# Kernel optimization log

Measured on AMD Instinct MI355X. Metric: run time of the kernel, lower is better.

Reference implementation:

```python
import jax, jax.numpy as jnp
import numpy as np

EPS = 1e-5

def _layernorm(x, g, b):
    m = jnp.mean(x, axis=-1, keepdims=True)
    v = jnp.var(x, axis=-1, keepdims=True)
    return (x - m) * jax.lax.rsqrt(v + EPS) * g + b

def setup_inputs() -> dict:
    key = jax.random.key(0)
    ks = jax.random.split(key, 8)
    B, N, D, H = 4, 2048, 1024, 16
    F = 2 * D
    s = 0.02
    return {
        "x": jax.random.normal(ks[0], (B, N, D), jnp.float32),
        "mask": jnp.zeros((B, N, N), jnp.float32),
        "Wq": jax.random.normal(ks[1], (D, D), jnp.float32) * s,
        "Wk": jax.random.normal(ks[2], (D, D), jnp.float32) * s,
        "Wv": jax.random.normal(ks[3], (D, D), jnp.float32) * s,
        "Wc": jax.random.normal(ks[4], (D, D), jnp.float32) * s,
        "bc": jnp.zeros((D,), jnp.float32),
        "W1": jax.random.normal(ks[5], (D, F), jnp.float32) * s,
        "b1": jnp.zeros((F,), jnp.float32),
        "W2": jax.random.normal(ks[6], (F, D), jnp.float32) * s,
        "b2": jnp.zeros((D,), jnp.float32),
        "g1": jnp.ones((D,), jnp.float32),
        "be1": jnp.zeros((D,), jnp.float32),
        "g2": jnp.ones((D,), jnp.float32),
        "be2": jnp.zeros((D,), jnp.float32),
    }

def reference(x, mask, Wq, Wk, Wv, Wc, bc, W1, b1, W2, b2, g1, be1, g2, be2):
    B, N, D = x.shape
    H = 16
    Dh = D // H
    scale = 1.0 / np.sqrt(Dh).astype(np.float32)
    # projections -> [B, H, N, Dh]
    def heads(t):
        return t.reshape(B, N, H, Dh).transpose(0, 2, 1, 3)
    q = heads(x @ Wq)
    k = heads(x @ Wk)
    v = heads(x @ Wv)
    score = jnp.einsum('bhnd,bhmd->bhnm', q, k) * scale + mask[:, None, :, :]
    attn = jnp.einsum('bhnm,bhmd->bhnd', jax.nn.softmax(score, axis=-1), v)
    attn = attn.transpose(0, 2, 1, 3).reshape(B, N, D)
    x = x + attn @ Wc + bc
    x = _layernorm(x, g1, be1)
    x = x + jnp.maximum(x @ W1 + b1, 0.0) @ W2 + b2
    x = _layernorm(x, g2, be2)
    return x
```

## Files before the change

kernel.cpp:

```cpp
#include <hip/hip_runtime.h>
#include <hip/hip_bf16.h>


#define DEV __device__ __forceinline__

using s16x8 = __attribute__((ext_vector_type(8))) short;
using f32x4 = __attribute__((ext_vector_type(4))) float;

DEV unsigned short f2bf(float f) {
  unsigned u = __float_as_uint(f);
  u += 0x7fffu + ((u >> 16) & 1u);
  return (unsigned short)(u >> 16);
}
DEV unsigned pack2bf(float a, float b) {
  return (unsigned)f2bf(a) | ((unsigned)f2bf(b) << 16);
}
DEV unsigned cvt_pk_bf16(float lo, float hi) {
  unsigned r;
  asm("v_cvt_pk_bf16_f32 %0, %1, %2" : "=v"(r) : "v"(lo), "v"(hi));
  return r;
}
DEV f32x4 vmax4(f32x4 a, f32x4 b) {
  f32x4 r;
  r[0] = fmaxf(a[0], b[0]); r[1] = fmaxf(a[1], b[1]);
  r[2] = fmaxf(a[2], b[2]); r[3] = fmaxf(a[3], b[3]);
  return r;
}

typedef __attribute__((address_space(3))) unsigned lds_u32_t;
typedef const __attribute__((address_space(1))) unsigned glb_u32_t;

DEV void gld_lds16(const void* g, void* l) {
  __builtin_amdgcn_global_load_lds((glb_u32_t*)g, (lds_u32_t*)l, 16, 0, 0);
}

template<int RELU, int VOUT>
__global__ __launch_bounds__(512, 2)
void gemm8p(const unsigned short* __restrict__ A, const unsigned short* __restrict__ Bt,
            unsigned short* __restrict__ Cb, const float* __restrict__ bias,
            unsigned short* __restrict__ vtout, int M, int N, int K)
{
  __shared__ unsigned short Sh[2][2][256 * 64];
  const int tid = threadIdx.x;
  const int w = tid >> 6, lane = tid & 63;
  const int g = lane >> 4, q = lane & 15;
  const int wr = w >> 2, wc = w & 3;

  const int nwg  = gridDim.x * gridDim.y;
  const int flat = blockIdx.y * gridDim.x + blockIdx.x;
  const int rm   = (flat & 7) * (nwg >> 3) + (flat >> 3);
  const int m0 = (rm / gridDim.x) * 256, n0 = (rm % gridDim.x) * 256;

  f32x4 acc[8][4] = {};

  const int srow = w * 8 + (lane >> 3);
  const int scol = ((lane & 7) ^ (lane >> 3)) * 8;
  const unsigned short* Ag = A  + (size_t)(m0 + srow) * K + scol;
  const unsigned short* Bg = Bt + (size_t)(n0 + srow) * K + scol;

  auto STG = [&](const unsigned short* Gb, int buf, int ab, int half, int kt) {
    const unsigned short* gs = Gb + (size_t)(half * 128) * K + kt * 64;
    unsigned short* ls = &Sh[buf][ab][(half * 128 + w * 8) * 64];
    gld_lds16(gs, ls);
    gld_lds16(gs + (size_t)64 * K, ls + 64 * 64);
  };
  auto LDA = [&](int buf, int mq, s16x8 af[4][2]) {
#pragma unroll
    for (int mm = 0; mm < 4; ++mm) {
      const unsigned short* rp = &Sh[buf][0][(wr * 128 + mq * 64 + mm * 16 + q) * 64];
#pragma unroll
      for (int kk = 0; kk < 2; ++kk)
        af[mm][kk] = *(const s16x8*)(rp + (((kk * 4 + g) ^ (q & 7)) * 8));
    }
  };
  auto LDB = [&](int buf, int nq, s16x8 bf[2][2]) {
#pragma unroll
    for (int nn = 0; nn < 2; ++nn) {
      const unsigned short* rp = &Sh[buf][1][(wc * 64 + nq * 32 + nn * 16 + q) * 64];
#pragma unroll
      for (int kk = 0; kk < 2; ++kk)
        bf[nn][kk] = *(const s16x8*)(rp + (((kk * 4 + g) ^ (q & 7)) * 8));
    }
  };
  auto MQ = [&](int mq, int nq, const s16x8 af[4][2], const s16x8 bf[2][2]) {
    __builtin_amdgcn_s_setprio(1);
#pragma unroll
    for (int kk = 0; kk < 2; ++kk)
#pragma unroll
      for (int mm = 0; mm < 4; ++mm)
#pragma unroll
        for (int nn = 0; nn < 2; ++nn)
          acc[mq * 4 + mm][nq * 2 + nn] = __builtin_amdgcn_mfma_f32_16x16x32_bf16(
              af[mm][kk], bf[nn][kk], acc[mq * 4 + mm][nq * 2 + nn], 0, 0, 0);
    __builtin_amdgcn_s_setprio(0);
  };
  auto BAR = [&]() { __builtin_amdgcn_sched_barrier(0); __builtin_amdgcn_s_barrier(); };

  STG(Ag, 0, 0, 0, 0); STG(Ag, 0, 0, 1, 0);
  STG(Bg, 0, 1, 0, 0); STG(Bg, 0, 1, 1, 0);

  const int NKT = K >> 6;
  s16x8 af[4][2], bf0[2][2], bf1[2][2];
#pragma unroll 1
  for (int kt = 0; kt < NKT; ++kt) {
    const int b = kt & 1, sb = b ^ 1, kn = kt + 1;
    const bool stg = (kn < NKT);
    if (stg) { STG(Ag, sb, 0, 0, kn); asm volatile("s_waitcnt vmcnt(2)" ::: "memory"); }
    else     {                        asm volatile("s_waitcnt vmcnt(0)" ::: "memory"); }
    BAR();
    LDA(b, 0, af); LDB(b, 0, bf0);
    MQ(0, 0, af, bf0);
    BAR();
    if (stg) STG(Ag, sb, 0, 1, kn);
    LDB(b, 1, bf1);
    MQ(0, 1, af, bf1);
    BAR();
    if (stg) STG(Bg, sb, 1, 0, kn);
    LDA(b, 1, af);
    MQ(1, 0, af, bf0);
    BAR();
    if (stg) STG(Bg, sb, 1, 1, kn);
    MQ(1, 1, af, bf1);
    BAR();
  }

#pragma unroll
  for (int n = 0; n < 4; ++n) {
    const int col = n0 + wc * 64 + n * 16 + q;
    if (VOUT && col >= 2048) {
      const int cv = col - 2048;
#pragma unroll
      for (int m = 0; m < 8; ++m) {
        const int row0 = m0 + wr * 128 + m * 16 + g * 4;
        const int bb = row0 >> 11;
        ushort4 pk;
        pk.x = f2bf(acc[m][n][0]); pk.y = f2bf(acc[m][n][1]);
        pk.z = f2bf(acc[m][n][2]); pk.w = f2bf(acc[m][n][3]);
        *(ushort4*)(vtout + ((size_t)bb * 1024 + cv) * 2048 + (row0 & 2047)) = pk;
      }
    } else {
      const float bv = bias ? bias[col] : 0.0f;
#pragma unroll
      for (int m = 0; m < 8; ++m) {
        const int row0 = m0 + wr * 128 + m * 16 + g * 4;
#pragma unroll
        for (int r = 0; r < 4; ++r) {
          float v = acc[m][n][r] + bv;
          if (RELU) v = fmaxf(v, 0.0f);
          Cb[(size_t)(row0 + r) * N + col] = f2bf(v);
        }
      }
    }
  }
}

template<int RELU, int RESID, int OUTF>
__global__ __launch_bounds__(256)
void gemm_bt(const unsigned short* __restrict__ A, const unsigned short* __restrict__ Bt,
             unsigned short* __restrict__ Cb, float* __restrict__ Cf,
             const float* __restrict__ bias, const float* __restrict__ resid,
             int M, int N, int K)
{
  __shared__ unsigned short As[128 * 32];
  __shared__ unsigned short Bs[128 * 32];
  const int tid  = threadIdx.x;
  const int wave = tid >> 6, lane = tid & 63;
  const int g = lane >> 4, q = lane & 15;

  const int nwg  = gridDim.x * gridDim.y;
  const int flat = blockIdx.y * gridDim.x + blockIdx.x;
  const int rm   = (nwg & 7) ? flat : ((flat & 7) * (nwg >> 3) + (flat >> 3));
  const int m0 = (rm / gridDim.x) * 128, n0 = (rm % gridDim.x) * 128;
  const int wr = wave >> 1, wc = wave & 1;

  f32x4 acc[4][4] = {};

  const int i0 = wave * 512 + lane * 8;
  const int i1 = 2048 + i0;

  for (int kt = 0; kt < K; kt += 32) {
    gld_lds16(A  + (size_t)(m0 + (i0 >> 5)) * K + kt + (i0 & 31), As + wave * 512);
    gld_lds16(Bt + (size_t)(n0 + (i0 >> 5)) * K + kt + (i0 & 31), Bs + wave * 512);
    gld_lds16(A  + (size_t)(m0 + (i1 >> 5)) * K + kt + (i1 & 31), As + 2048 + wave * 512);
    gld_lds16(Bt + (size_t)(n0 + (i1 >> 5)) * K + kt + (i1 & 31), Bs + 2048 + wave * 512);
    __syncthreads();
    s16x8 a[4], b[4];
#pragma unroll
    for (int m = 0; m < 4; ++m)
      a[m] = *(const s16x8*)(As + (wr * 64 + m * 16 + q) * 32 + g * 8);
#pragma unroll
    for (int n = 0; n < 4; ++n)
      b[n] = *(const s16x8*)(Bs + (wc * 64 + n * 16 + q) * 32 + g * 8);
#pragma unroll
    for (int m = 0; m < 4; ++m)
#pragma unroll
      for (int n = 0; n < 4; ++n)
        acc[m][n] = __builtin_amdgcn_mfma_f32_16x16x32_bf16(a[m], b[n], acc[m][n], 0, 0, 0);
    __syncthreads();
  }

#pragma unroll
  for (int n = 0; n < 4; ++n) {
    const int col = n0 + wc * 64 + n * 16 + q;
    const float bv = bias ? bias[col] : 0.0f;
#pragma unroll
    for (int m = 0; m < 4; ++m) {
      const int row0 = m0 + wr * 64 + m * 16 + g * 4;
#pragma unroll
      for (int r = 0; r < 4; ++r) {
        float v = acc[m][n][r] + bv;
        if (RELU) v = fmaxf(v, 0.0f);
        if (RESID) v += resid[(size_t)(row0 + r) * N + col];
        if (OUTF) Cf[(size_t)(row0 + r) * N + col] = v;
        else      Cb[(size_t)(row0 + r) * N + col] = f2bf(v);
      }
    }
  }
}

__global__ __launch_bounds__(256, 4)
void attn_kernel(const unsigned short* __restrict__ qkv,
                 const unsigned short* __restrict__ vt,
                 const float* __restrict__ mask,
                 unsigned short* __restrict__ outb)
{
  __shared__ unsigned short Ks[2][4096];
  __shared__ unsigned short Vs[2][4096];
  __shared__ unsigned short Pl[4][1024];
  const int tid = threadIdx.x, wave = tid >> 6, lane = tid & 63;
  const int g = lane >> 4, q = lane & 15;

  const int flat = blockIdx.y * 32 + blockIdx.x;
  const int rm   = (flat & 7) * 256 + (flat >> 3);
  const int qt = rm & 31, bh = rm >> 5;
  const int b = bh >> 4, h = bh & 15;
  const int qrow = qt * 64 + wave * 16;
  const size_t tok0 = (size_t)b * 2048;

  const unsigned short* Qp = qkv + (tok0 + qrow + q) * 3072 + h * 64;
  const s16x8 bq0 = *(const s16x8*)(Qp + g * 8);
  const s16x8 bq1 = *(const s16x8*)(Qp + 32 + g * 8);
  const float* Mp = mask + ((size_t)b * 2048 + qrow + q) * 2048;

  const int lr = lane >> 3;
  const int sc = (lane & 7) ^ lr;
  const unsigned short* Kg = qkv + tok0 * 3072 + 1024 + h * 64
                           + (size_t)(wave * 16 + lr) * 3072 + sc * 8;
  const unsigned short* Vg = vt + ((size_t)bh * 64 + wave * 16 + lr) * 2048 + sc * 8;
  unsigned short* KsW = Ks[0] + wave * 1024;
  unsigned short* VsW = Vs[0] + wave * 1024;

  auto STAGE = [&](int buf, int t) {
    const size_t ko = (size_t)t * (64 * 3072);
    const int    vo = t * 64;
    gld_lds16(Kg + ko,            KsW + buf * 4096);
    gld_lds16(Kg + ko + 8 * 3072, KsW + buf * 4096 + 512);
    gld_lds16(Vg + vo,            VsW + buf * 4096);
    gld_lds16(Vg + vo + 8 * 2048, VsW + buf * 4096 + 512);
  };

  f32x4 ot[4] = {};
  f32x4 mkc[4], mkn[4];
  float mrun = -3.0e38f, mnl = 0.0f, lsum = 0.0f;
  char* Pw = (char*)&Pl[wave][0];
  const float SC  = 0.125f;
  const float L2E = 1.4426950408889634f;

  STAGE(0, 0);
#pragma unroll
  for (int m2 = 0; m2 < 4; ++m2) mkc[m2] = *(const f32x4*)(Mp + m2 * 16 + g * 4);
  __syncthreads();

  int cur = 0;
#pragma unroll 1
  for (int t = 0; t < 32; ++t) {
    if (t < 31) {
      STAGE(cur ^ 1, t + 1);
#pragma unroll
      for (int m2 = 0; m2 < 4; ++m2)
        mkn[m2] = *(const f32x4*)(Mp + (t + 1) * 64 + m2 * 16 + g * 4);
    }
    const unsigned short* Kt = Ks[cur];
    const unsigned short* Vt = Vs[cur];

    f32x4 st[4] = {};
    __builtin_amdgcn_s_setprio(1);
#pragma unroll
    for (int m2 = 0; m2 < 4; ++m2) {
      const unsigned short* kp = Kt + (m2 * 16 + q) * 64;
      const s16x8 ak0 = *(const s16x8*)(kp + ((g       ^ (q & 7)) * 8));
      const s16x8 ak1 = *(const s16x8*)(kp + (((g + 4) ^ (q & 7)) * 8));
      st[m2] = __builtin_amdgcn_mfma_f32_16x16x32_bf16(ak0, bq0, st[m2], 0, 0, 0);
      st[m2] = __builtin_amdgcn_mfma_f32_16x16x32_bf16(ak1, bq1, st[m2], 0, 0, 0);
    }
    __builtin_amdgcn_s_setprio(0);

#pragma unroll
    for (int m2 = 0; m2 < 4; ++m2)
#pragma unroll
      for (int r = 0; r < 4; ++r)
        st[m2][r] = fmaf(st[m2][r], SC, mkc[m2][r]);

    f32x4 a0 = vmax4(vmax4(st[0], st[1]), vmax4(st[2], st[3]));
    float tmax = fmaxf(fmaxf(a0[0], a0[1]), fmaxf(a0[2], a0[3]));
    tmax = fmaxf(tmax, __shfl_xor(tmax, 16));
    tmax = fmaxf(tmax, __shfl_xor(tmax, 32));

    if (!__all(tmax <= mrun + 8.0f)) {
      const float mn = fmaxf(mrun, tmax);
      const float al = exp2f((mrun - mn) * L2E);
      mrun = mn; mnl = mn * L2E;
      lsum *= al;
#pragma unroll
      for (int m = 0; m < 4; ++m) {
        ot[m][0] *= al; ot[m][1] *= al; ot[m][2] *= al; ot[m][3] *= al;
      }
    }

    float rsum = 0.0f;
#pragma unroll
    for (int m2 = 0; m2 < 4; ++m2) {
#pragma unroll
      for (int r = 0; r < 4; ++r)
        st[m2][r] = exp2f(fmaf(st[m2][r], L2E, -mnl));
      rsum += (st[m2][0] + st[m2][1]) + (st[m2][2] + st[m2][3]);
      const int bir  = m2 * 32 + g * 8;
      const int addr = q * 128 + (((bir >> 4) ^ (q & 7)) << 4) + (bir & 15);
      uint2 pk;
      pk.x = cvt_pk_bf16(st[m2][0], st[m2][1]);
      pk.y = cvt_pk_bf16(st[m2][2], st[m2][3]);
      *(uint2*)(Pw + addr) = pk;
    }
    rsum += __shfl_xor(rsum, 16);
    rsum += __shfl_xor(rsum, 32);
    lsum += rsum;

    __builtin_amdgcn_s_setprio(1);
#pragma unroll
    for (int kb = 0; kb < 2; ++kb) {
      const int blk = (kb * 4 + g) ^ (q & 7);
      const s16x8 pb = *(const s16x8*)(Pw + q * 128 + blk * 16);
#pragma unroll
      for (int m = 0; m < 4; ++m) {
        const s16x8 av = *(const s16x8*)(Vt + (m * 16 + q) * 64 + blk * 8);
        ot[m] = __builtin_amdgcn_mfma_f32_16x16x32_bf16(av, pb, ot[m], 0, 0, 0);
      }
    }
    __builtin_amdgcn_s_setprio(0);

#pragma unroll
    for (int m2 = 0; m2 < 4; ++m2) mkc[m2] = mkn[m2];
    __syncthreads();
    cur ^= 1;
  }

  const float inv = 1.0f / lsum;
#pragma unroll
  for (int m = 0; m < 4; ++m) {
    const int bir  = m * 32 + g * 8;
    const int addr = q * 128 + (((bir >> 4) ^ (q & 7)) << 4) + (bir & 15);
    uint2 pk;
    pk.x = cvt_pk_bf16(ot[m][0] * inv, ot[m][1] * inv);
    pk.y = cvt_pk_bf16(ot[m][2] * inv, ot[m][3] * inv);
    *(uint2*)(Pw + addr) = pk;
  }
#pragma unroll
  for (int p = 0; p < 2; ++p) {
    const int c  = p * 64 + lane;
    const int qq = c >> 3, cc = c & 7;
    const int blk = cc ^ (qq & 7);
    const s16x8 vv = *(const s16x8*)(Pw + qq * 128 + blk * 16);
    *(s16x8*)(outb + (tok0 + qrow + qq) * 1024 + h * 64 + cc * 8) = vv;
  }
}

__global__ __launch_bounds__(256)
void ln_kernel(const float* __restrict__ in, float* __restrict__ outf,
               unsigned short* __restrict__ outb,
               const float* __restrict__ gam, const float* __restrict__ bet)
{
  __shared__ float red[8];
  const int row = blockIdx.x, tid = threadIdx.x;
  const f32x4 v = *(const f32x4*)(in + (size_t)row * 1024 + tid * 4);
  float s  = v[0] + v[1] + v[2] + v[3];
  float ss = v[0]*v[0] + v[1]*v[1] + v[2]*v[2] + v[3]*v[3];
#pragma unroll
  for (int o = 1; o < 64; o <<= 1) { s += __shfl_xor(s, o); ss += __shfl_xor(ss, o); }
  if ((tid & 63) == 0) { red[tid >> 6] = s; red[4 + (tid >> 6)] = ss; }
  __syncthreads();
  s  = red[0] + red[1] + red[2] + red[3];
  ss = red[4] + red[5] + red[6] + red[7];
  const float mean = s * (1.0f / 1024.0f);
  const float var  = ss * (1.0f / 1024.0f) - mean * mean;
  const float rstd = rsqrtf(var + 1e-5f);
  const f32x4 gm = *(const f32x4*)(gam + tid * 4);
  const f32x4 bt = *(const f32x4*)(bet + tid * 4);
  f32x4 o;
#pragma unroll
  for (int j = 0; j < 4; ++j) o[j] = (v[j] - mean) * rstd * gm[j] + bt[j];
  if (outf) *(f32x4*)(outf + (size_t)row * 1024 + tid * 4) = o;
  if (outb) {
    uint2 pk; pk.x = pack2bf(o[0], o[1]); pk.y = pack2bf(o[2], o[3]);
    *(uint2*)(outb + (size_t)row * 1024 + tid * 4) = pk;
  }
}

__global__ __launch_bounds__(256)
void tcast_kernel(const float* __restrict__ in, unsigned short* __restrict__ out, int R, int C)
{
  __shared__ float t[32][33];
  const int tx = threadIdx.x & 31, ty = threadIdx.x >> 5;
  const int c0 = blockIdx.x * 32, r0 = blockIdx.y * 32;
#pragma unroll
  for (int k = 0; k < 4; ++k)
    t[ty + k * 8][tx] = in[(size_t)(r0 + ty + k * 8) * C + c0 + tx];
  __syncthreads();
#pragma unroll
  for (int k = 0; k < 4; ++k)
    out[(size_t)(c0 + ty + k * 8) * R + r0 + tx] = f2bf(t[tx][ty + k * 8]);
}

__global__ __launch_bounds__(256)
void cast_x_kernel(const float* __restrict__ in, unsigned short* __restrict__ out)
{
  const size_t i = ((size_t)blockIdx.x * 256 + threadIdx.x) * 4;
  const f32x4 v = *(const f32x4*)(in + i);
  uint2 pk; pk.x = pack2bf(v[0], v[1]); pk.y = pack2bf(v[2], v[3]);
  *(uint2*)(out + i) = pk;
}

extern "C" void kernel_launch(void* const* d_in, const int* in_sizes, int n_in,
                              void* d_out, int out_size, void* d_ws, size_t ws_size,
                              hipStream_t stream)
{
  (void)in_sizes; (void)n_in; (void)out_size; (void)ws_size;
  const float* x   = (const float*)d_in[0];
  const float* msk = (const float*)d_in[1];
  const float* Wq  = (const float*)d_in[2];
  const float* Wk  = (const float*)d_in[3];
  const float* Wv  = (const float*)d_in[4];
  const float* Wc  = (const float*)d_in[5];
  const float* bc  = (const float*)d_in[6];
  const float* W1  = (const float*)d_in[7];
  const float* b1  = (const float*)d_in[8];
  const float* W2  = (const float*)d_in[9];
  const float* b2  = (const float*)d_in[10];
  const float* g1  = (const float*)d_in[11];
  const float* be1 = (const float*)d_in[12];
  const float* g2  = (const float*)d_in[13];
  const float* be2 = (const float*)d_in[14];
  float* out = (float*)d_out;
  char* ws = (char*)d_ws;
  const size_t MB = 1u << 20;
  unsigned short* xb    = (unsigned short*)(ws + 0 * MB);
  unsigned short* wqkvt = (unsigned short*)(ws + 16 * MB);
  unsigned short* wct   = (unsigned short*)(ws + 22 * MB);
  unsigned short* w1t   = (unsigned short*)(ws + 24 * MB);
  unsigned short* w2t   = (unsigned short*)(ws + 28 * MB);
  unsigned short* qkv   = (unsigned short*)(ws + 32 * MB);
  unsigned short* vt    = (unsigned short*)(ws + 80 * MB);
  unsigned short* attnb = xb;
  float*          y1    = (float*)(ws + 32 * MB);
  unsigned short* h1b   = (unsigned short*)(ws + 64 * MB);
  float*          h1f   = (float*)(ws + 96 * MB);
  unsigned short* midb  = (unsigned short*)(ws + 128 * MB);

  cast_x_kernel<<<8192, 256, 0, stream>>>(x, xb);
  tcast_kernel<<<dim3(32, 32), 256, 0, stream>>>(Wq, wqkvt,               1024, 1024);
  tcast_kernel<<<dim3(32, 32), 256, 0, stream>>>(Wk, wqkvt + 1024 * 1024, 1024, 1024);
  tcast_kernel<<<dim3(32, 32), 256, 0, stream>>>(Wv, wqkvt + 2048 * 1024, 1024, 1024);
  tcast_kernel<<<dim3(32, 32), 256, 0, stream>>>(Wc, wct,                 1024, 1024);
  tcast_kernel<<<dim3(64, 32), 256, 0, stream>>>(W1, w1t,                 1024, 2048);
  tcast_kernel<<<dim3(32, 64), 256, 0, stream>>>(W2, w2t,                 2048, 1024);

  gemm8p<0, 1><<<dim3(12, 32), 512, 0, stream>>>(xb, wqkvt, qkv, nullptr, vt,
                                                 8192, 3072, 1024);
  attn_kernel<<<dim3(32, 64), 256, 0, stream>>>(qkv, vt, msk, attnb);
  gemm_bt<0, 1, 1><<<dim3(8, 64), 256, 0, stream>>>(attnb, wct, nullptr, y1,
                                                    bc, x, 8192, 1024, 1024);
  ln_kernel<<<8192, 256, 0, stream>>>(y1, h1f, h1b, g1, be1);
  gemm8p<1, 0><<<dim3(8, 32), 512, 0, stream>>>(h1b, w1t, midb, b1, nullptr,
                                                8192, 2048, 1024);
  gemm_bt<0, 1, 1><<<dim3(8, 64), 256, 0, stream>>>(midb, w2t, nullptr, out,
                                                    b2, h1f, 8192, 1024, 2048);
  ln_kernel<<<8192, 256, 0, stream>>>(out, out, nullptr, g2, be2);
}
```

Measured before the change: 453.7 us.

## Use bf16 intermediates for residual/LN path and fold softmax scale into Q projection

Several changes land together. Residual-add GEMM outputs and the LayerNorm inputs now use bf16 instead of fp32, and the residuals are read from the bf16 copies of x and h1, which cuts the memory traffic of the elementwise and epilogue stages. The attention scale and log2(e) are folded into the Q projection epilogue, and the row sum of the softmax is computed by an MFMA against a ones vector instead of shuffle reductions. Software bf16 packing is also replaced by the hardware cvt_pk instruction. Numerical precision drops because residuals and pre-LN activations are rounded to bf16, and the rescale threshold changes.

```diff
diff --git a/kernel.cpp b/kernel.cpp
--- a/kernel.cpp
+++ b/kernel.cpp
@@ -12,20 +12,12 @@
   u += 0x7fffu + ((u >> 16) & 1u);
   return (unsigned short)(u >> 16);
 }
-DEV unsigned pack2bf(float a, float b) {
-  return (unsigned)f2bf(a) | ((unsigned)f2bf(b) << 16);
-}
 DEV unsigned cvt_pk_bf16(float lo, float hi) {
   unsigned r;
   asm("v_cvt_pk_bf16_f32 %0, %1, %2" : "=v"(r) : "v"(lo), "v"(hi));
   return r;
 }
-DEV f32x4 vmax4(f32x4 a, f32x4 b) {
-  f32x4 r;
-  r[0] = fmaxf(a[0], b[0]); r[1] = fmaxf(a[1], b[1]);
-  r[2] = fmaxf(a[2], b[2]); r[3] = fmaxf(a[3], b[3]);
-  return r;
-}
+DEV float bf2f(unsigned short b) { return __uint_as_float((unsigned)b << 16); }
 
 typedef __attribute__((address_space(3))) unsigned lds_u32_t;
 typedef const __attribute__((address_space(1))) unsigned glb_u32_t;
@@ -139,13 +131,14 @@
         *(ushort4*)(vtout + ((size_t)bb * 1024 + cv) * 2048 + (row0 & 2047)) = pk;
       }
     } else {
+      const float scl = (VOUT && col < 1024) ? 0.18033688011112042f : 1.0f;
       const float bv = bias ? bias[col] : 0.0f;
 #pragma unroll
       for (int m = 0; m < 8; ++m) {
         const int row0 = m0 + wr * 128 + m * 16 + g * 4;
 #pragma unroll
         for (int r = 0; r < 4; ++r) {
-          float v = acc[m][n][r] + bv;
+          float v = acc[m][n][r] * scl + bv;
           if (RELU) v = fmaxf(v, 0.0f);
           Cb[(size_t)(row0 + r) * N + col] = f2bf(v);
         }
@@ -159,6 +152,7 @@
 void gemm_bt(const unsigned short* __restrict__ A, const unsigned short* __restrict__ Bt,
              unsigned short* __restrict__ Cb, float* __restrict__ Cf,
              const float* __restrict__ bias, const float* __restrict__ resid,
+             const unsigned short* __restrict__ residb,
              int M, int N, int K)
 {
   __shared__ unsigned short As[128 * 32];
@@ -210,7 +204,8 @@
       for (int r = 0; r < 4; ++r) {
         float v = acc[m][n][r] + bv;
         if (RELU) v = fmaxf(v, 0.0f);
-        if (RESID) v += resid[(size_t)(row0 + r) * N + col];
+        if (RESID == 1) v += resid[(size_t)(row0 + r) * N + col];
+        if (RESID == 2) v += bf2f(residb[(size_t)(row0 + r) * N + col]);
         if (OUTF) Cf[(size_t)(row0 + r) * N + col] = v;
         else      Cb[(size_t)(row0 + r) * N + col] = f2bf(v);
       }
@@ -259,12 +254,17 @@
     gld_lds16(Vg + vo + 8 * 2048, VsW + buf * 4096 + 512);
   };
 
+  s16x8 ones;
+#pragma unroll
+  for (int j = 0; j < 8; ++j) ones[j] = (short)0x3F80;
+
   f32x4 ot[4] = {};
+  f32x4 sacc = {};
   f32x4 mkc[4], mkn[4];
-  float mrun = -3.0e38f, mnl = 0.0f, lsum = 0.0f;
+  float m = -3.0e38f;
   char* Pw = (char*)&Pl[wave][0];
-  const float SC  = 0.125f;
   const float L2E = 1.4426950408889634f;
+  const float THR = 11.541560327111707f;
 
   STAGE(0, 0);
 #pragma unroll
@@ -299,31 +299,32 @@
     for (int m2 = 0; m2 < 4; ++m2)
 #pragma unroll
       for (int r = 0; r < 4; ++r)
-        st[m2][r] = fmaf(st[m2][r], SC, mkc[m2][r]);
-
-    f32x4 a0 = vmax4(vmax4(st[0], st[1]), vmax4(st[2], st[3]));
-    float tmax = fmaxf(fmaxf(a0[0], a0[1]), fmaxf(a0[2], a0[3]));
+        st[m2][r] = fmaf(mkc[m2][r], L2E, st[m2][r]);
+
+    float c0 = fmaxf(fmaxf(fmaxf(st[0][0], st[0][1]), st[0][2]), st[0][3]);
+    float c1 = fmaxf(fmaxf(fmaxf(st[1][0], st[1][1]), st[1][2]), st[1][3]);
+    float c2 = fmaxf(fmaxf(fmaxf(st[2][0], st[2][1]), st[2][2]), st[2][3]);
+    float c3 = fmaxf(fmaxf(fmaxf(st[3][0], st[3][1]), st[3][2]), st[3][3]);
+    float tmax = fmaxf(fmaxf(fmaxf(c0, c1), c2), c3);
     tmax = fmaxf(tmax, __shfl_xor(tmax, 16));
     tmax = fmaxf(tmax, __shfl_xor(tmax, 32));
 
-    if (!__all(tmax <= mrun + 8.0f)) {
-      const float mn = fmaxf(mrun, tmax);
-      const float al = exp2f((mrun - mn) * L2E);
-      mrun = mn; mnl = mn * L2E;
-      lsum *= al;
-#pragma unroll
-      for (int m = 0; m < 4; ++m) {
-        ot[m][0] *= al; ot[m][1] *= al; ot[m][2] *= al; ot[m][3] *= al;
+    if (!__all(tmax <= m + THR)) {
+      const float mn = fmaxf(m, tmax);
+      const float al = exp2f(m - mn);
+      m = mn;
+      sacc[0] *= al;
+#pragma unroll
+      for (int mm = 0; mm < 4; ++mm) {
+        ot[mm][0] *= al; ot[mm][1] *= al; ot[mm][2] *= al; ot[mm][3] *= al;
       }
     }
 
-    float rsum = 0.0f;
 #pragma unroll
     for (int m2 = 0; m2 < 4; ++m2) {
 #pragma unroll
       for (int r = 0; r < 4; ++r)
-        st[m2][r] = exp2f(fmaf(st[m2][r], L2E, -mnl));
-      rsum += (st[m2][0] + st[m2][1]) + (st[m2][2] + st[m2][3]);
+        st[m2][r] = exp2f(st[m2][r] - m);
       const int bir  = m2 * 32 + g * 8;
       const int addr = q * 128 + (((bir >> 4) ^ (q & 7)) << 4) + (bir & 15);
       uint2 pk;
@@ -331,19 +332,17 @@
       pk.y = cvt_pk_bf16(st[m2][2], st[m2][3]);
       *(uint2*)(Pw + addr) = pk;
     }
-    rsum += __shfl_xor(rsum, 16);
-    rsum += __shfl_xor(rsum, 32);
-    lsum += rsum;
 
     __builtin_amdgcn_s_setprio(1);
 #pragma unroll
     for (int kb = 0; kb < 2; ++kb) {
       const int blk = (kb * 4 + g) ^ (q & 7);
       const s16x8 pb = *(const s16x8*)(Pw + q * 128 + blk * 16);
-#pragma unroll
-      for (int m = 0; m < 4; ++m) {
-        const s16x8 av = *(const s16x8*)(Vt + (m * 16 + q) * 64 + blk * 8);
-        ot[m] = __builtin_amdgcn_mfma_f32_16x16x32_bf16(av, pb, ot[m], 0, 0, 0);
+      sacc = __builtin_amdgcn_mfma_f32_16x16x32_bf16(ones, pb, sacc, 0, 0, 0);
+#pragma unroll
+      for (int mm = 0; mm < 4; ++mm) {
+        const s16x8 av = *(const s16x8*)(Vt + (mm * 16 + q) * 64 + blk * 8);
+        ot[mm] = __builtin_amdgcn_mfma_f32_16x16x32_bf16(av, pb, ot[mm], 0, 0, 0);
       }
     }
     __builtin_amdgcn_s_setprio(0);
@@ -354,14 +353,14 @@
     cur ^= 1;
   }
 
-  const float inv = 1.0f / lsum;
-#pragma unroll
-  for (int m = 0; m < 4; ++m) {
-    const int bir  = m * 32 + g * 8;
+  const float inv = 1.0f / sacc[0];
+#pragma unroll
+  for (int mm = 0; mm < 4; ++mm) {
+    const int bir  = mm * 32 + g * 8;
     const int addr = q * 128 + (((bir >> 4) ^ (q & 7)) << 4) + (bir & 15);
     uint2 pk;
-    pk.x = cvt_pk_bf16(ot[m][0] * inv, ot[m][1] * inv);
-    pk.y = cvt_pk_bf16(ot[m][2] * inv, ot[m][3] * inv);
+    pk.x = cvt_pk_bf16(ot[mm][0] * inv, ot[mm][1] * inv);
+    pk.y = cvt_pk_bf16(ot[mm][2] * inv, ot[mm][3] * inv);
     *(uint2*)(Pw + addr) = pk;
   }
 #pragma unroll
@@ -374,14 +373,22 @@
   }
 }
 
+template<int INBF>
 __global__ __launch_bounds__(256)
-void ln_kernel(const float* __restrict__ in, float* __restrict__ outf,
-               unsigned short* __restrict__ outb,
+void ln_kernel(const float* __restrict__ inf, const unsigned short* __restrict__ inb,
+               float* __restrict__ outf, unsigned short* __restrict__ outb,
                const float* __restrict__ gam, const float* __restrict__ bet)
 {
   __shared__ float red[8];
   const int row = blockIdx.x, tid = threadIdx.x;
-  const f32x4 v = *(const f32x4*)(in + (size_t)row * 1024 + tid * 4);
+  f32x4 v;
+  if (INBF) {
+    const uint2 u = *(const uint2*)(inb + (size_t)row * 1024 + tid * 4);
+    v[0] = __uint_as_float(u.x << 16); v[1] = __uint_as_float(u.x & 0xffff0000u);
+    v[2] = __uint_as_float(u.y << 16); v[3] = __uint_as_float(u.y & 0xffff0000u);
+  } else {
+    v = *(const f32x4*)(inf + (size_t)row * 1024 + tid * 4);
+  }
   float s  = v[0] + v[1] + v[2] + v[3];
   float ss = v[0]*v[0] + v[1]*v[1] + v[2]*v[2] + v[3]*v[3];
 #pragma unroll
@@ -400,7 +407,7 @@
   for (int j = 0; j < 4; ++j) o[j] = (v[j] - mean) * rstd * gm[j] + bt[j];
   if (outf) *(f32x4*)(outf + (size_t)row * 1024 + tid * 4) = o;
   if (outb) {
-    uint2 pk; pk.x = pack2bf(o[0], o[1]); pk.y = pack2bf(o[2], o[3]);
+    uint2 pk; pk.x = cvt_pk_bf16(o[0], o[1]); pk.y = cvt_pk_bf16(o[2], o[3]);
     *(uint2*)(outb + (size_t)row * 1024 + tid * 4) = pk;
   }
 }
@@ -425,7 +432,7 @@
 {
   const size_t i = ((size_t)blockIdx.x * 256 + threadIdx.x) * 4;
   const f32x4 v = *(const f32x4*)(in + i);
-  uint2 pk; pk.x = pack2bf(v[0], v[1]); pk.y = pack2bf(v[2], v[3]);
+  uint2 pk; pk.x = cvt_pk_bf16(v[0], v[1]); pk.y = cvt_pk_bf16(v[2], v[3]);
   *(uint2*)(out + i) = pk;
 }
 
@@ -459,11 +466,11 @@
   unsigned short* w2t   = (unsigned short*)(ws + 28 * MB);
   unsigned short* qkv   = (unsigned short*)(ws + 32 * MB);
   unsigned short* vt    = (unsigned short*)(ws + 80 * MB);
-  unsigned short* attnb = xb;
-  float*          y1    = (float*)(ws + 32 * MB);
-  unsigned short* h1b   = (unsigned short*)(ws + 64 * MB);
-  float*          h1f   = (float*)(ws + 96 * MB);
-  unsigned short* midb  = (unsigned short*)(ws + 128 * MB);
+  unsigned short* attnb = (unsigned short*)(ws + 96 * MB);
+  unsigned short* y1b   = (unsigned short*)(ws + 112 * MB);
+  unsigned short* midb  = (unsigned short*)(ws + 32 * MB);
+  unsigned short* z2b   = (unsigned short*)(ws + 64 * MB);
+  unsigned short* h1b   = (unsigned short*)(ws + 128 * MB);
 
   cast_x_kernel<<<8192, 256, 0, stream>>>(x, xb);
   tcast_kernel<<<dim3(32, 32), 256, 0, stream>>>(Wq, wqkvt,               1024, 1024);
@@ -476,12 +483,12 @@
   gemm8p<0, 1><<<dim3(12, 32), 512, 0, stream>>>(xb, wqkvt, qkv, nullptr, vt,
                                                  8192, 3072, 1024);
   attn_kernel<<<dim3(32, 64), 256, 0, stream>>>(qkv, vt, msk, attnb);
-  gemm_bt<0, 1, 1><<<dim3(8, 64), 256, 0, stream>>>(attnb, wct, nullptr, y1,
-                                                    bc, x, 8192, 1024, 1024);
-  ln_kernel<<<8192, 256, 0, stream>>>(y1, h1f, h1b, g1, be1);
+  gemm_bt<0, 2, 0><<<dim3(8, 64), 256, 0, stream>>>(attnb, wct, y1b, nullptr,
+                                                    bc, nullptr, xb, 8192, 1024, 1024);
+  ln_kernel<1><<<8192, 256, 0, stream>>>(nullptr, y1b, nullptr, h1b, g1, be1);
   gemm8p<1, 0><<<dim3(8, 32), 512, 0, stream>>>(h1b, w1t, midb, b1, nullptr,
                                                 8192, 2048, 1024);
-  gemm_bt<0, 1, 1><<<dim3(8, 64), 256, 0, stream>>>(midb, w2t, nullptr, out,
-                                                    b2, h1f, 8192, 1024, 2048);
-  ln_kernel<<<8192, 256, 0, stream>>>(out, out, nullptr, g2, be2);
-}
+  gemm_bt<0, 2, 0><<<dim3(8, 64), 256, 0, stream>>>(midb, w2t, z2b, nullptr,
+                                                    b2, nullptr, h1b, 8192, 1024, 2048);
+  ln_kernel<1><<<8192, 256, 0, stream>>>(nullptr, z2b, out, nullptr, g2, be2);
+}
```

New measurement: 432.1 us. -4.8%, faster.
